# Performance work log

Measured on AMD Instinct MI355X. Metric: run time of the kernel, lower is better.

Reference implementation:

```python
import jax, jax.numpy as jnp
import numpy as np

N_NODES = 100000
N_EDGES = 1600000
D = 128          # in_channels // 4
IN_CH = 512
OUT_CH = 256
NUM_LABELS = 4


def setup_inputs() -> dict:
    key = jax.random.key(0)
    k1, k2, k3, k4, k5, k6 = jax.random.split(key, 6)
    x = jax.random.normal(k1, (N_NODES, D), dtype=jnp.float32)
    edge_index = jax.random.randint(k2, (2, N_EDGES), 0, N_NODES, dtype=jnp.int64)
    edge_label = jax.random.uniform(k3, (N_EDGES, NUM_LABELS), dtype=jnp.float32)
    # Parameters (uniform init per module's reset_parameters)
    stdv_w = 1.0 / np.sqrt(IN_CH)
    stdv_t = 1.0 / np.sqrt(NUM_LABELS)
    weight = jax.random.uniform(k4, (IN_CH, OUT_CH), minval=-stdv_w, maxval=stdv_w, dtype=jnp.float32)
    trans_weight = jax.random.uniform(k5, (NUM_LABELS, D), minval=-stdv_t, maxval=stdv_t, dtype=jnp.float32)
    bias = jax.random.uniform(k6, (OUT_CH,), minval=-stdv_w, maxval=stdv_w, dtype=jnp.float32)
    return {"x": x, "edge_index": edge_index, "edge_label": edge_label,
            "weight": weight, "trans_weight": trans_weight, "bias": bias}


def _scatter_mean(vals, idx, num_segments):
    # segment mean; empty segments -> 0 (matches torch_scatter.scatter_mean)
    s = jax.ops.segment_sum(vals, idx, num_segments=num_segments)
    cnt = jax.ops.segment_sum(jnp.ones((vals.shape[0],), dtype=vals.dtype), idx,
                              num_segments=num_segments)
    return s / jnp.maximum(cnt, 1.0)[:, None]


def reference(x, edge_index, edge_label, weight, trans_weight, bias):
    row, col = edge_index[0], edge_index[1]
    n = x.shape[0]
    # edge-label transform: [E, L] @ [L, D] -> [E, D]
    elt = jnp.matmul(edge_label, trans_weight)
    opinion = _scatter_mean(elt, row, n)        # outgoing opinion aggregation
    out = _scatter_mean(x[col], row, n)          # outgoing neighbor features
    inn_opinion = _scatter_mean(elt, col, n)     # incoming opinion aggregation
    inn = _scatter_mean(x[row], col, n)          # incoming neighbor features
    h = jnp.concatenate((out, opinion, inn, inn_opinion), axis=1)  # [N, 4D]
    return jnp.matmul(h, weight) + bias
```

## Files before the change

kernel.cpp:

```cpp
#include <hip/hip_runtime.h>
#include <hip/hip_bf16.h>


#define BK 64
#define BKSH 6
#define CHUNK 4096
#define CAPSEG 2048
#define CSSH 11
#define NB_CVT 256

typedef unsigned short u16;
typedef unsigned long long u64;
typedef __attribute__((ext_vector_type(4))) float f32x4;
typedef __attribute__((ext_vector_type(8))) short bf16x8;

__device__ inline unsigned pk_bf16(float a, float b) {
    __hip_bfloat162 h;
    h.x = __float2bfloat16(a);
    h.y = __float2bfloat16(b);
    return *reinterpret_cast<unsigned*>(&h);
}
__device__ inline float2 upk_bf16(unsigned u) {
    __hip_bfloat162 h = *reinterpret_cast<__hip_bfloat162*>(&u);
    return make_float2(__bfloat162float(h.x), __bfloat162float(h.y));
}
__device__ inline u16 f2bf(float f) {
    __hip_bfloat16 h = __float2bfloat16(f);
    return *reinterpret_cast<u16*>(&h);
}

__global__ __launch_bounds__(256) void cvt_bin(
    const float2* __restrict__ x2, unsigned* __restrict__ xh,
    const int* __restrict__ eidx, const float4* __restrict__ elab4,
    int* __restrict__ cnt_r, int* __restrict__ cnt_c,
    uint2* __restrict__ ent_r, uint2* __restrict__ ent_c,
    const float* __restrict__ w, const float* __restrict__ tw,
    u16* __restrict__ wb, int n2, int E, int nbk, int nchunk)
{
    __shared__ int smem[2048];
    const int t = threadIdx.x;
    const unsigned bid = blockIdx.x;

    if (bid < 2u * nchunk) {
        int* cB = smem;
        const int dir = (bid >= (unsigned)nchunk);
        const int base = (dir ? bid - nchunk : bid) * CHUNK;
        const int* __restrict__ osrc = eidx + (dir ? (size_t)E : 0);
        const int* __restrict__ psrc = eidx + (dir ? 0 : (size_t)E);
        int* __restrict__ cnt = dir ? cnt_c : cnt_r;
        uint2* __restrict__ ent = dir ? ent_c : ent_r;

        for (int i = t; i < nbk; i += 256) cB[i] = 0;
        __syncthreads();

        int4 own4[4], par4[4];
        unsigned lq[16];
        bool ok[4];
        #pragma unroll
        for (int jj = 0; jj < 4; ++jj) {
            const int e0 = base + (jj * 256 + t) * 4;
            ok[jj] = (e0 < E);
            if (ok[jj]) {
                own4[jj] = *(const int4*)(osrc + e0);
                par4[jj] = *(const int4*)(psrc + e0);
                #pragma unroll
                for (int k = 0; k < 4; ++k) {
                    const float4 lb = elab4[e0 + k];
                    const unsigned q0 = (unsigned)(lb.x * 255.f + 0.5f);
                    const unsigned q1 = (unsigned)(lb.y * 255.f + 0.5f);
                    const unsigned q2 = (unsigned)(lb.z * 255.f + 0.5f);
                    const unsigned q3 = (unsigned)(lb.w * 255.f + 0.5f);
                    lq[jj * 4 + k] = q0 | (q1 << 8) | (q2 << 16) | (q3 << 24);
                }
                atomicAdd(&cB[((unsigned)own4[jj].x) >> BKSH], 1);
                atomicAdd(&cB[((unsigned)own4[jj].y) >> BKSH], 1);
                atomicAdd(&cB[((unsigned)own4[jj].z) >> BKSH], 1);
                atomicAdd(&cB[((unsigned)own4[jj].w) >> BKSH], 1);
            }
        }
        __syncthreads();
        for (int b = t; b < nbk; b += 256) {
            const int c = cB[b];
            cB[b] = c ? ((b << CSSH) + atomicAdd(&cnt[b], c)) : 0;
        }
        __syncthreads();
        #pragma unroll
        for (int jj = 0; jj < 4; ++jj) {
            if (ok[jj]) {
                const int owns[4] = {own4[jj].x, own4[jj].y, own4[jj].z, own4[jj].w};
                const int pars[4] = {par4[jj].x, par4[jj].y, par4[jj].z, par4[jj].w};
                #pragma unroll
                for (int k = 0; k < 4; ++k) {
                    const unsigned own = (unsigned)owns[k];
                    const int p = atomicAdd(&cB[own >> BKSH], 1);
                    ent[p] = make_uint2((unsigned)pars[k] | ((own & (BK - 1u)) << 17),
                                        lq[jj * 4 + k]);
                }
            }
        }
        return;
    }

    if (bid < 2u * nchunk + NB_CVT) {
        const int cb = bid - 2 * nchunk;
        const int gsz = NB_CVT * 256;
        for (int i = cb * 256 + t; i < n2; i += gsz) {
            const float2 v = x2[i];
            xh[i] = pk_bf16(v.x, v.y);
        }
        return;
    }

    float (*P)[256] = (float(*)[256])smem;
    const int pid0 = (bid - 2 * nchunk - NB_CVT) * 256;
    if (pid0 + 255 >= 8192) {
        for (int q = t; q < 2048; q += 256) {
            const int l = q >> 8;
            const int cidx = q & 255;
            const int lr = l & 3;
            const int off = (l < 4) ? 128 : 384;
            float s = 0.f;
            for (int c = 0; c < 128; ++c)
                s = fmaf(tw[lr * 128 + c], w[(size_t)(off + c) * 256 + cidx], s);
            P[l][cidx] = s;
        }
        __syncthreads();
    }
    const int pid = pid0 + t;
    if (pid >= 9 * 16 * 64) return;
    const int ks = pid >> 10;
    const int ct = (pid >> 6) & 15;
    const int l  = pid & 63;
    const int col = ct * 16 + (l & 15);
    const int k0 = ks * 32 + ((l >> 4) << 3);
    u16 v[8];
    #pragma unroll
    for (int j = 0; j < 8; ++j) {
        const int k = k0 + j;
        float f = 0.f;
        if (k < 128)      f = w[(size_t)k * 256 + col];
        else if (k < 256) f = w[(size_t)(k + 128) * 256 + col];
        else if (k < 264) f = P[k - 256][col];
        v[j] = f2bf(f);
    }
    *(uint4*)(wb + (size_t)pid * 8) = *(uint4*)v;
}

__device__ inline void addrow(float* acc, const uint4 r) {
    const float2 a = upk_bf16(r.x), b = upk_bf16(r.y),
                 c = upk_bf16(r.z), d = upk_bf16(r.w);
    acc[0] += a.x; acc[1] += a.y; acc[2] += b.x; acc[3] += b.y;
    acc[4] += c.x; acc[5] += c.y; acc[6] += d.x; acc[7] += d.y;
}

__global__ __launch_bounds__(256) void sort_accum(
    const uint2* __restrict__ ent1_r, const uint2* __restrict__ ent1_c,
    const int* __restrict__ cnt_r, const int* __restrict__ cnt_c,
    const uint4* __restrict__ xh4,
    uint4* __restrict__ om4, uint4* __restrict__ im4,
    u16* __restrict__ lab_h, int nn, int nbk)
{
    __shared__ unsigned sorted[CAPSEG];
    __shared__ int hist[BK], sc[BK], curs[BK];
    __shared__ u64 labacc[BK];
    const int t = threadIdx.x;
    const int dir = (blockIdx.x >= (unsigned)nbk);
    const int b = blockIdx.x - (dir ? nbk : 0);
    const uint2* __restrict__ buf1 = (dir ? ent1_c : ent1_r) + ((size_t)b << CSSH);
    uint4* __restrict__ mean4 = dir ? im4 : om4;
    int cnt = (dir ? cnt_c : cnt_r)[b];
    if (cnt > CAPSEG) cnt = CAPSEG;

    if (t < BK) { hist[t] = 0; labacc[t] = 0ull; }
    __syncthreads();
    for (int i = t; i < cnt; i += 256) {
        const uint2 en = buf1[i];
        const unsigned local = en.x >> 17;
        atomicAdd(&hist[local], 1);
        const unsigned lv = en.y;
        const u64 spread = (u64)(lv & 255u) | ((u64)((lv >> 8) & 255u) << 16)
                         | ((u64)((lv >> 16) & 255u) << 32) | ((u64)(lv >> 24) << 48);
        atomicAdd(&labacc[local], spread);
    }
    __syncthreads();
    if (t < BK) sc[t] = hist[t];
    __syncthreads();
    for (int s = 1; s < BK; s <<= 1) {
        int v = 0;
        if (t < BK && t >= s) v = sc[t - s];
        __syncthreads();
        if (t < BK) sc[t] += v;
        __syncthreads();
    }
    if (t < BK) {
        curs[t] = sc[t] - hist[t];
        const int gn = b * BK + t;
        if (gn < nn) {
            const u64 sv = labacc[t];
            const float inv = (1.f / 255.f) / fmaxf((float)hist[t], 1.f);
            u16 lm[4];
            #pragma unroll
            for (int l = 0; l < 4; ++l)
                lm[l] = f2bf((float)((sv >> (16 * l)) & 0xFFFFu) * inv);
            *(uint2*)(lab_h + (size_t)gn * 8 + dir * 4) = *(uint2*)lm;
        }
    }
    __syncthreads();
    for (int i = t; i < cnt; i += 256) {
        const uint2 en = buf1[i];
        const int p = atomicAdd(&curs[en.x >> 17], 1);
        sorted[p] = en.x & 0x1FFFFu;
    }
    __syncthreads();

    const int wid = t >> 6;
    const int lane = t & 63;
    const int g = lane >> 4;
    const int sl = lane & 15;
    for (int local = wid; local < BK; local += 4) {
        const int gn = b * BK + local;
        if (gn >= nn) continue;
        const int segC = hist[local];
        const int segS = sc[local] - segC;
        float acc[8] = {0.f, 0.f, 0.f, 0.f, 0.f, 0.f, 0.f, 0.f};
        for (int i = 0; i < segC; i += 16) {
            const int rem = segC - i;
            const bool h0 = (g < rem);
            const bool h1 = (g + 4 < rem);
            const bool h2 = (g + 8 < rem);
            const bool h3 = (g + 12 < rem);
            const unsigned p0 = h0 ? sorted[segS + i + g] : 0u;
            const unsigned p1 = h1 ? sorted[segS + i + 4 + g] : 0u;
            const unsigned p2 = h2 ? sorted[segS + i + 8 + g] : 0u;
            const unsigned p3 = h3 ? sorted[segS + i + 12 + g] : 0u;
            uint4 r0, r1, r2, r3;
            if (h0) r0 = xh4[(size_t)p0 * 16 + sl];
            if (h1) r1 = xh4[(size_t)p1 * 16 + sl];
            if (h2) r2 = xh4[(size_t)p2 * 16 + sl];
            if (h3) r3 = xh4[(size_t)p3 * 16 + sl];
            if (h0) addrow(acc, r0);
            if (h1) addrow(acc, r1);
            if (h2) addrow(acc, r2);
            if (h3) addrow(acc, r3);
        }
        #pragma unroll
        for (int j = 0; j < 8; ++j) {
            acc[j] += __shfl_xor(acc[j], 16);
            acc[j] += __shfl_xor(acc[j], 32);
        }
        if (g == 0) {
            const float inv = 1.0f / fmaxf((float)segC, 1.0f);
            uint4 o;
            o.x = pk_bf16(acc[0] * inv, acc[1] * inv);
            o.y = pk_bf16(acc[2] * inv, acc[3] * inv);
            o.z = pk_bf16(acc[4] * inv, acc[5] * inv);
            o.w = pk_bf16(acc[6] * inv, acc[7] * inv);
            mean4[(size_t)gn * 16 + sl] = o;
        }
    }
}

__global__ __launch_bounds__(256) void gemm_mfma(
    const u16* __restrict__ om_h, const u16* __restrict__ im_h,
    const u16* __restrict__ lab_h, const u16* __restrict__ wb,
    const float* __restrict__ bias, float* __restrict__ out, int nn)
{
    const int t = threadIdx.x;
    const int w = t >> 6;
    const int lane = t & 63;
    const int m15 = lane & 15;
    const int kq  = lane >> 4;
    const int node0 = blockIdx.x * 64;

    f32x4 acc[4][4];
    #pragma unroll
    for (int i = 0; i < 4; ++i)
        #pragma unroll
        for (int j = 0; j < 4; ++j)
            acc[i][j] = (f32x4){0.f, 0.f, 0.f, 0.f};

    for (int ks = 0; ks < 9; ++ks) {
        const int k0 = ks * 32 + kq * 8;
        bf16x8 af[4], bfr[4];
        #pragma unroll
        for (int nt = 0; nt < 4; ++nt) {
            const int gn = node0 + nt * 16 + m15;
            bf16x8 a = (bf16x8){0, 0, 0, 0, 0, 0, 0, 0};
            if (gn < nn && k0 < 264) {
                const u16* p = (k0 < 128) ? om_h + (size_t)gn * 128 + k0
                             : (k0 < 256) ? im_h + (size_t)gn * 128 + (k0 - 128)
                                          : lab_h + (size_t)gn * 8;
                a = *(const bf16x8*)p;
            }
            af[nt] = a;
        }
        #pragma unroll
        for (int c2 = 0; c2 < 4; ++c2)
            bfr[c2] = *(const bf16x8*)(wb + ((size_t)((ks * 16 + w * 4 + c2) * 64 + lane)) * 8);
        #pragma unroll
        for (int nt = 0; nt < 4; ++nt)
            #pragma unroll
            for (int c2 = 0; c2 < 4; ++c2)
                acc[nt][c2] = __builtin_amdgcn_mfma_f32_16x16x32_bf16(
                    af[nt], bfr[c2], acc[nt][c2], 0, 0, 0);
    }

    #pragma unroll
    for (int nt = 0; nt < 4; ++nt) {
        const int gnb = node0 + nt * 16 + kq * 4;
        #pragma unroll
        for (int c2 = 0; c2 < 4; ++c2) {
            const int oc = w * 64 + c2 * 16 + m15;
            const float bv = bias[oc];
            #pragma unroll
            for (int r = 0; r < 4; ++r) {
                const int gn = gnb + r;
                if (gn < nn)
                    __builtin_nontemporal_store(acc[nt][c2][r] + bv,
                                                &out[(size_t)gn * 256 + oc]);
            }
        }
    }
}

extern "C" void kernel_launch(void* const* d_in, const int* in_sizes, int n_in,
                              void* d_out, int out_size, void* d_ws, size_t ws_size,
                              hipStream_t stream) {
    const float* x      = (const float*)d_in[0];
    const int*   eidx   = (const int*)d_in[1];
    const float* elabel = (const float*)d_in[2];
    const float* weight = (const float*)d_in[3];
    const float* tw     = (const float*)d_in[4];
    const float* bias   = (const float*)d_in[5];

    const int n = in_sizes[0] / 128;
    const int E = in_sizes[2] / 4;
    const int nbk = (n + BK - 1) / BK;
    const int nchunk = (E + CHUNK - 1) / CHUNK;

    char* wsb = (char*)d_ws;
    u16* om_h    = (u16*)wsb;   wsb += (size_t)n * 256;
    u16* im_h    = (u16*)wsb;   wsb += (size_t)n * 256;
    u16* lab_h   = (u16*)wsb;   wsb += (size_t)n * 16;
    u16* wb      = (u16*)wsb;   wsb += 9216 * 16;
    int* cnt_r   = (int*)wsb;   wsb += nbk * 4;
    int* cnt_c   = (int*)wsb;   wsb += nbk * 4;

    unsigned* xh = (unsigned*)d_out;
    uint2* ent1_r = (uint2*)(xh + (size_t)n * 64);
    uint2* ent1_c = ent1_r + ((size_t)nbk << CSSH);

    hipMemsetAsync(cnt_r, 0, (size_t)2 * nbk * sizeof(int), stream);

    hipLaunchKernelGGL(cvt_bin, dim3(2 * nchunk + NB_CVT + 36), dim3(256), 0, stream,
                       (const float2*)x, xh, eidx, (const float4*)elabel,
                       cnt_r, cnt_c, ent1_r, ent1_c,
                       weight, tw, wb, n * 64, E, nbk, nchunk);

    hipLaunchKernelGGL(sort_accum, dim3(2 * nbk), dim3(256), 0, stream,
                       ent1_r, ent1_c, cnt_r, cnt_c, (const uint4*)xh,
                       (uint4*)om_h, (uint4*)im_h, lab_h, n, nbk);

    hipLaunchKernelGGL(gemm_mfma, dim3((n + 63) / 64), dim3(256), 0, stream,
                       om_h, im_h, lab_h, wb, bias, (float*)d_out, n);
}
```

Before: 271.7 us.

## Fuse sort-accumulate and MFMA GEMM into one kernel via LDS staging

Merges the segment-mean aggregation kernel and the GEMM kernel into a single kernel. Each block now handles both edge directions for its 64 nodes, keeps the bf16 means and label means in shared memory, and then runs the MFMA GEMM straight from LDS. This removes the global write and re-read of the om/im/lab intermediates and one kernel launch. In exchange it halves the grid, serializes the two directions within a block, and raises LDS use, which can lower occupancy. Scratch buffers move from the output buffer to the workspace because the output is now written in the same kernel.

```diff
diff --git a/kernel.cpp b/kernel.cpp
--- a/kernel.cpp
+++ b/kernel.cpp
@@ -8,6 +8,7 @@
 #define CAPSEG 2048
 #define CSSH 11
 #define NB_CVT 256
+#define LDM 136
 
 typedef unsigned short u16;
 typedef unsigned long long u64;
@@ -153,125 +154,120 @@
     acc[4] += c.x; acc[5] += c.y; acc[6] += d.x; acc[7] += d.y;
 }
 
-__global__ __launch_bounds__(256) void sort_accum(
+__global__ __launch_bounds__(256) void sag(
     const uint2* __restrict__ ent1_r, const uint2* __restrict__ ent1_c,
     const int* __restrict__ cnt_r, const int* __restrict__ cnt_c,
-    const uint4* __restrict__ xh4,
-    uint4* __restrict__ om4, uint4* __restrict__ im4,
-    u16* __restrict__ lab_h, int nn, int nbk)
+    const uint4* __restrict__ xh4, const u16* __restrict__ wb,
+    const float* __restrict__ bias, float* __restrict__ out, int nn)
 {
     __shared__ unsigned sorted[CAPSEG];
     __shared__ int hist[BK], sc[BK], curs[BK];
     __shared__ u64 labacc[BK];
+    __shared__ u16 om_lds[BK * LDM];
+    __shared__ u16 im_lds[BK * LDM];
+    __shared__ u16 lab_lds[BK * 8];
     const int t = threadIdx.x;
-    const int dir = (blockIdx.x >= (unsigned)nbk);
-    const int b = blockIdx.x - (dir ? nbk : 0);
-    const uint2* __restrict__ buf1 = (dir ? ent1_c : ent1_r) + ((size_t)b << CSSH);
-    uint4* __restrict__ mean4 = dir ? im4 : om4;
-    int cnt = (dir ? cnt_c : cnt_r)[b];
-    if (cnt > CAPSEG) cnt = CAPSEG;
-
-    if (t < BK) { hist[t] = 0; labacc[t] = 0ull; }
-    __syncthreads();
-    for (int i = t; i < cnt; i += 256) {
-        const uint2 en = buf1[i];
-        const unsigned local = en.x >> 17;
-        atomicAdd(&hist[local], 1);
-        const unsigned lv = en.y;
-        const u64 spread = (u64)(lv & 255u) | ((u64)((lv >> 8) & 255u) << 16)
-                         | ((u64)((lv >> 16) & 255u) << 32) | ((u64)(lv >> 24) << 48);
-        atomicAdd(&labacc[local], spread);
-    }
-    __syncthreads();
-    if (t < BK) sc[t] = hist[t];
-    __syncthreads();
-    for (int s = 1; s < BK; s <<= 1) {
-        int v = 0;
-        if (t < BK && t >= s) v = sc[t - s];
-        __syncthreads();
-        if (t < BK) sc[t] += v;
-        __syncthreads();
-    }
-    if (t < BK) {
-        curs[t] = sc[t] - hist[t];
-        const int gn = b * BK + t;
-        if (gn < nn) {
-            const u64 sv = labacc[t];
-            const float inv = (1.f / 255.f) / fmaxf((float)hist[t], 1.f);
-            u16 lm[4];
-            #pragma unroll
-            for (int l = 0; l < 4; ++l)
-                lm[l] = f2bf((float)((sv >> (16 * l)) & 0xFFFFu) * inv);
-            *(uint2*)(lab_h + (size_t)gn * 8 + dir * 4) = *(uint2*)lm;
-        }
-    }
-    __syncthreads();
-    for (int i = t; i < cnt; i += 256) {
-        const uint2 en = buf1[i];
-        const int p = atomicAdd(&curs[en.x >> 17], 1);
-        sorted[p] = en.x & 0x1FFFFu;
-    }
-    __syncthreads();
-
+    const int b = blockIdx.x;
     const int wid = t >> 6;
     const int lane = t & 63;
     const int g = lane >> 4;
     const int sl = lane & 15;
-    for (int local = wid; local < BK; local += 4) {
-        const int gn = b * BK + local;
-        if (gn >= nn) continue;
-        const int segC = hist[local];
-        const int segS = sc[local] - segC;
-        float acc[8] = {0.f, 0.f, 0.f, 0.f, 0.f, 0.f, 0.f, 0.f};
-        for (int i = 0; i < segC; i += 16) {
-            const int rem = segC - i;
-            const bool h0 = (g < rem);
-            const bool h1 = (g + 4 < rem);
-            const bool h2 = (g + 8 < rem);
-            const bool h3 = (g + 12 < rem);
-            const unsigned p0 = h0 ? sorted[segS + i + g] : 0u;
-            const unsigned p1 = h1 ? sorted[segS + i + 4 + g] : 0u;
-            const unsigned p2 = h2 ? sorted[segS + i + 8 + g] : 0u;
-            const unsigned p3 = h3 ? sorted[segS + i + 12 + g] : 0u;
-            uint4 r0, r1, r2, r3;
-            if (h0) r0 = xh4[(size_t)p0 * 16 + sl];
-            if (h1) r1 = xh4[(size_t)p1 * 16 + sl];
-            if (h2) r2 = xh4[(size_t)p2 * 16 + sl];
-            if (h3) r3 = xh4[(size_t)p3 * 16 + sl];
-            if (h0) addrow(acc, r0);
-            if (h1) addrow(acc, r1);
-            if (h2) addrow(acc, r2);
-            if (h3) addrow(acc, r3);
-        }
-        #pragma unroll
-        for (int j = 0; j < 8; ++j) {
-            acc[j] += __shfl_xor(acc[j], 16);
-            acc[j] += __shfl_xor(acc[j], 32);
-        }
-        if (g == 0) {
-            const float inv = 1.0f / fmaxf((float)segC, 1.0f);
-            uint4 o;
-            o.x = pk_bf16(acc[0] * inv, acc[1] * inv);
-            o.y = pk_bf16(acc[2] * inv, acc[3] * inv);
-            o.z = pk_bf16(acc[4] * inv, acc[5] * inv);
-            o.w = pk_bf16(acc[6] * inv, acc[7] * inv);
-            mean4[(size_t)gn * 16 + sl] = o;
-        }
-    }
-}
-
-__global__ __launch_bounds__(256) void gemm_mfma(
-    const u16* __restrict__ om_h, const u16* __restrict__ im_h,
-    const u16* __restrict__ lab_h, const u16* __restrict__ wb,
-    const float* __restrict__ bias, float* __restrict__ out, int nn)
-{
-    const int t = threadIdx.x;
-    const int w = t >> 6;
-    const int lane = t & 63;
+    const int node0 = b * BK;
+
+    for (int dir = 0; dir < 2; ++dir) {
+        const uint2* __restrict__ buf1 = (dir ? ent1_c : ent1_r) + ((size_t)b << CSSH);
+        u16* __restrict__ mean_lds = dir ? im_lds : om_lds;
+        int cnt = (dir ? cnt_c : cnt_r)[b];
+        if (cnt > CAPSEG) cnt = CAPSEG;
+
+        if (t < BK) { hist[t] = 0; labacc[t] = 0ull; }
+        __syncthreads();
+        for (int i = t; i < cnt; i += 256) {
+            const uint2 en = buf1[i];
+            const unsigned local = en.x >> 17;
+            atomicAdd(&hist[local], 1);
+            const unsigned lv = en.y;
+            const u64 spread = (u64)(lv & 255u) | ((u64)((lv >> 8) & 255u) << 16)
+                             | ((u64)((lv >> 16) & 255u) << 32) | ((u64)(lv >> 24) << 48);
+            atomicAdd(&labacc[local], spread);
+        }
+        __syncthreads();
+        if (t < BK) sc[t] = hist[t];
+        __syncthreads();
+        for (int s = 1; s < BK; s <<= 1) {
+            int v = 0;
+            if (t < BK && t >= s) v = sc[t - s];
+            __syncthreads();
+            if (t < BK) sc[t] += v;
+            __syncthreads();
+        }
+        if (t < BK) {
+            curs[t] = sc[t] - hist[t];
+            const int gn = node0 + t;
+            if (gn < nn) {
+                const u64 sv = labacc[t];
+                const float inv = (1.f / 255.f) / fmaxf((float)hist[t], 1.f);
+                u16 lm[4];
+                #pragma unroll
+                for (int l = 0; l < 4; ++l)
+                    lm[l] = f2bf((float)((sv >> (16 * l)) & 0xFFFFu) * inv);
+                *(uint2*)(&lab_lds[t * 8 + dir * 4]) = *(uint2*)lm;
+            }
+        }
+        __syncthreads();
+        for (int i = t; i < cnt; i += 256) {
+            const uint2 en = buf1[i];
+            const int p = atomicAdd(&curs[en.x >> 17], 1);
+            sorted[p] = en.x & 0x1FFFFu;
+        }
+        __syncthreads();
+
+        for (int local = wid; local < BK; local += 4) {
+            const int gn = node0 + local;
+            if (gn >= nn) continue;
+            const int segC = hist[local];
+            const int segS = sc[local] - segC;
+            float acc[8] = {0.f, 0.f, 0.f, 0.f, 0.f, 0.f, 0.f, 0.f};
+            for (int i = 0; i < segC; i += 16) {
+                const int rem = segC - i;
+                const bool h0 = (g < rem);
+                const bool h1 = (g + 4 < rem);
+                const bool h2 = (g + 8 < rem);
+                const bool h3 = (g + 12 < rem);
+                const unsigned p0 = h0 ? sorted[segS + i + g] : 0u;
+                const unsigned p1 = h1 ? sorted[segS + i + 4 + g] : 0u;
+                const unsigned p2 = h2 ? sorted[segS + i + 8 + g] : 0u;
+                const unsigned p3 = h3 ? sorted[segS + i + 12 + g] : 0u;
+                uint4 r0, r1, r2, r3;
+                if (h0) r0 = xh4[(size_t)p0 * 16 + sl];
+                if (h1) r1 = xh4[(size_t)p1 * 16 + sl];
+                if (h2) r2 = xh4[(size_t)p2 * 16 + sl];
+                if (h3) r3 = xh4[(size_t)p3 * 16 + sl];
+                if (h0) addrow(acc, r0);
+                if (h1) addrow(acc, r1);
+                if (h2) addrow(acc, r2);
+                if (h3) addrow(acc, r3);
+            }
+            #pragma unroll
+            for (int j = 0; j < 8; ++j) {
+                acc[j] += __shfl_xor(acc[j], 16);
+                acc[j] += __shfl_xor(acc[j], 32);
+            }
+            if (g == 0) {
+                const float inv = 1.0f / fmaxf((float)segC, 1.0f);
+                uint4 o;
+                o.x = pk_bf16(acc[0] * inv, acc[1] * inv);
+                o.y = pk_bf16(acc[2] * inv, acc[3] * inv);
+                o.z = pk_bf16(acc[4] * inv, acc[5] * inv);
+                o.w = pk_bf16(acc[6] * inv, acc[7] * inv);
+                *(uint4*)(&mean_lds[local * LDM + sl * 8]) = o;
+            }
+        }
+        __syncthreads();
+    }
+
     const int m15 = lane & 15;
     const int kq  = lane >> 4;
-    const int node0 = blockIdx.x * 64;
-
     f32x4 acc[4][4];
     #pragma unroll
     for (int i = 0; i < 4; ++i)
@@ -284,19 +280,18 @@
         bf16x8 af[4], bfr[4];
         #pragma unroll
         for (int nt = 0; nt < 4; ++nt) {
-            const int gn = node0 + nt * 16 + m15;
+            const int row = nt * 16 + m15;
             bf16x8 a = (bf16x8){0, 0, 0, 0, 0, 0, 0, 0};
-            if (gn < nn && k0 < 264) {
-                const u16* p = (k0 < 128) ? om_h + (size_t)gn * 128 + k0
-                             : (k0 < 256) ? im_h + (size_t)gn * 128 + (k0 - 128)
-                                          : lab_h + (size_t)gn * 8;
-                a = *(const bf16x8*)p;
+            if (k0 < 264) {
+                if (k0 < 128)      a = *(const bf16x8*)(&om_lds[row * LDM + k0]);
+                else if (k0 < 256) a = *(const bf16x8*)(&im_lds[row * LDM + (k0 - 128)]);
+                else               a = *(const bf16x8*)(&lab_lds[row * 8]);
             }
             af[nt] = a;
         }
         #pragma unroll
         for (int c2 = 0; c2 < 4; ++c2)
-            bfr[c2] = *(const bf16x8*)(wb + ((size_t)((ks * 16 + w * 4 + c2) * 64 + lane)) * 8);
+            bfr[c2] = *(const bf16x8*)(wb + ((size_t)((ks * 16 + wid * 4 + c2) * 64 + lane)) * 8);
         #pragma unroll
         for (int nt = 0; nt < 4; ++nt)
             #pragma unroll
@@ -310,7 +305,7 @@
         const int gnb = node0 + nt * 16 + kq * 4;
         #pragma unroll
         for (int c2 = 0; c2 < 4; ++c2) {
-            const int oc = w * 64 + c2 * 16 + m15;
+            const int oc = wid * 64 + c2 * 16 + m15;
             const float bv = bias[oc];
             #pragma unroll
             for (int r = 0; r < 4; ++r) {
@@ -339,16 +334,12 @@
     const int nchunk = (E + CHUNK - 1) / CHUNK;
 
     char* wsb = (char*)d_ws;
-    u16* om_h    = (u16*)wsb;   wsb += (size_t)n * 256;
-    u16* im_h    = (u16*)wsb;   wsb += (size_t)n * 256;
-    u16* lab_h   = (u16*)wsb;   wsb += (size_t)n * 16;
-    u16* wb      = (u16*)wsb;   wsb += 9216 * 16;
-    int* cnt_r   = (int*)wsb;   wsb += nbk * 4;
-    int* cnt_c   = (int*)wsb;   wsb += nbk * 4;
-
-    unsigned* xh = (unsigned*)d_out;
-    uint2* ent1_r = (uint2*)(xh + (size_t)n * 64);
-    uint2* ent1_c = ent1_r + ((size_t)nbk << CSSH);
+    unsigned* xh  = (unsigned*)wsb;  wsb += (size_t)n * 256;
+    uint2* ent1_r = (uint2*)wsb;     wsb += ((size_t)nbk << CSSH) * 8;
+    uint2* ent1_c = (uint2*)wsb;     wsb += ((size_t)nbk << CSSH) * 8;
+    u16* wb       = (u16*)wsb;       wsb += 9216 * 16;
+    int* cnt_r    = (int*)wsb;       wsb += nbk * 4;
+    int* cnt_c    = (int*)wsb;       wsb += nbk * 4;
 
     hipMemsetAsync(cnt_r, 0, (size_t)2 * nbk * sizeof(int), stream);
 
@@ -357,10 +348,7 @@
                        cnt_r, cnt_c, ent1_r, ent1_c,
                        weight, tw, wb, n * 64, E, nbk, nchunk);
 
-    hipLaunchKernelGGL(sort_accum, dim3(2 * nbk), dim3(256), 0, stream,
+    hipLaunchKernelGGL(sag, dim3(nbk), dim3(256), 0, stream,
                        ent1_r, ent1_c, cnt_r, cnt_c, (const uint4*)xh,
-                       (uint4*)om_h, (uint4*)im_h, lab_h, n, nbk);
-
-    hipLaunchKernelGGL(gemm_mfma, dim3((n + 63) / 64), dim3(256), 0, stream,
-                       om_h, im_h, lab_h, wb, bias, (float*)d_out, n);
-}
+                       wb, bias, (float*)d_out, n);
+}
```

Result: slower. 350.0 us (+28.8%).

## Fuse GEMM into sort_accum via per-bucket completion flags, double bucket size

Applied to the files above, without the earlier changes.

Doubles the node bucket size (BK 64→128, segment capacity 2048→4096) and fuses the final MFMA GEMM into the sort/accumulate kernel. Each bucket's two direction blocks increment an atomic flag, and the second one to finish runs the GEMM for that bucket's 128 nodes. Staging buffers move from the output buffer into workspace when there is room, so output writes cannot clobber entries still being read. This removes a kernel launch and lets the GEMM overlap the scatter phase. The costs are fewer, larger sort blocks with more shared memory and a tail imbalance. It also relies on a fence and flag protocol, and `wid`/`lane` must be defined in the hidden part of sort_accum.

```diff
diff --git a/kernel.cpp b/kernel.cpp
--- a/kernel.cpp
+++ b/kernel.cpp
@@ -2,11 +2,11 @@
 #include <hip/hip_bf16.h>
 
 
-#define BK 64
-#define BKSH 6
+#define BK 128
+#define BKSH 7
 #define CHUNK 4096
-#define CAPSEG 2048
-#define CSSH 11
+#define CAPSEG 4096
+#define CSSH 12
 #define NB_CVT 256
 
 typedef unsigned short u16;
@@ -153,16 +153,78 @@
     acc[4] += c.x; acc[5] += c.y; acc[6] += d.x; acc[7] += d.y;
 }
 
+__device__ inline void gemm_tile(
+    int node0, const u16* __restrict__ om_h, const u16* __restrict__ im_h,
+    const u16* __restrict__ lab_h, const u16* __restrict__ wb,
+    const float* __restrict__ bias, float* __restrict__ out, int nn,
+    int wid, int lane)
+{
+    const int m15 = lane & 15;
+    const int kq  = lane >> 4;
+    f32x4 acc[4][4];
+    #pragma unroll
+    for (int i = 0; i < 4; ++i)
+        #pragma unroll
+        for (int j = 0; j < 4; ++j)
+            acc[i][j] = (f32x4){0.f, 0.f, 0.f, 0.f};
+
+    for (int ks = 0; ks < 9; ++ks) {
+        const int k0 = ks * 32 + kq * 8;
+        bf16x8 af[4], bfr[4];
+        #pragma unroll
+        for (int nt = 0; nt < 4; ++nt) {
+            const int gn = node0 + nt * 16 + m15;
+            bf16x8 a = (bf16x8){0, 0, 0, 0, 0, 0, 0, 0};
+            if (gn < nn && k0 < 264) {
+                const u16* p = (k0 < 128) ? om_h + (size_t)gn * 128 + k0
+                             : (k0 < 256) ? im_h + (size_t)gn * 128 + (k0 - 128)
+                                          : lab_h + (size_t)gn * 8;
+                a = *(const bf16x8*)p;
+            }
+            af[nt] = a;
+        }
+        #pragma unroll
+        for (int c2 = 0; c2 < 4; ++c2)
+            bfr[c2] = *(const bf16x8*)(wb + ((size_t)((ks * 16 + wid * 4 + c2) * 64 + lane)) * 8);
+        #pragma unroll
+        for (int nt = 0; nt < 4; ++nt)
+            #pragma unroll
+            for (int c2 = 0; c2 < 4; ++c2)
+                acc[nt][c2] = __builtin_amdgcn_mfma_f32_16x16x32_bf16(
+                    af[nt], bfr[c2], acc[nt][c2], 0, 0, 0);
+    }
+
+    #pragma unroll
+    for (int nt = 0; nt < 4; ++nt) {
+        const int gnb = node0 + nt * 16 + kq * 4;
+        #pragma unroll
+        for (int c2 = 0; c2 < 4; ++c2) {
+            const int oc = wid * 64 + c2 * 16 + m15;
+            const float bv = bias[oc];
+            #pragma unroll
+            for (int r = 0; r < 4; ++r) {
+                const int gn = gnb + r;
+                if (gn < nn)
+                    __builtin_nontemporal_store(acc[nt][c2][r] + bv,
+                                                &out[(size_t)gn * 256 + oc]);
+            }
+        }
+    }
+}
+
 __global__ __launch_bounds__(256) void sort_accum(
     const uint2* __restrict__ ent1_r, const uint2* __restrict__ ent1_c,
     const int* __restrict__ cnt_r, const int* __restrict__ cnt_c,
     const uint4* __restrict__ xh4,
     uint4* __restrict__ om4, uint4* __restrict__ im4,
-    u16* __restrict__ lab_h, int nn, int nbk)
+    u16* __restrict__ lab_h, int* __restrict__ flags,
+    const u16* __restrict__ wb, const float* __restrict__ bias,
+    float* __restrict__ out, int nn, int nbk, int fuse)
 {
     __shared__ unsigned sorted[CAPSEG];
     __shared__ int hist[BK], sc[BK], curs[BK];
     __shared__ u64 labacc[BK];
+    __shared__ int sflag;
     const int t = threadIdx.x;
     const int dir = (blockIdx.x >= (unsigned)nbk);
     const int b = blockIdx.x - (dir ? nbk : 0);
@@ -258,6 +320,22 @@
             mean4[(size_t)gn * 16 + sl] = o;
         }
     }
+
+    if (!fuse) return;
+
+    __syncthreads();
+    if (t == 0) {
+        __threadfence();
+        sflag = atomicAdd(&flags[b], 1);
+    }
+    __syncthreads();
+    if (sflag == 1) {
+        __threadfence();
+        gemm_tile(b * BK,      (const u16*)om4, (const u16*)im4, lab_h, wb,
+                  bias, out, nn, wid, lane);
+        gemm_tile(b * BK + 64, (const u16*)om4, (const u16*)im4, lab_h, wb,
+                  bias, out, nn, wid, lane);
+    }
 }
 
 __global__ __launch_bounds__(256) void gemm_mfma(
@@ -265,62 +343,8 @@
     const u16* __restrict__ lab_h, const u16* __restrict__ wb,
     const float* __restrict__ bias, float* __restrict__ out, int nn)
 {
-    const int t = threadIdx.x;
-    const int w = t >> 6;
-    const int lane = t & 63;
-    const int m15 = lane & 15;
-    const int kq  = lane >> 4;
-    const int node0 = blockIdx.x * 64;
-
-    f32x4 acc[4][4];
-    #pragma unroll
-    for (int i = 0; i < 4; ++i)
-        #pragma unroll
-        for (int j = 0; j < 4; ++j)
-            acc[i][j] = (f32x4){0.f, 0.f, 0.f, 0.f};
-
-    for (int ks = 0; ks < 9; ++ks) {
-        const int k0 = ks * 32 + kq * 8;
-        bf16x8 af[4], bfr[4];
-        #pragma unroll
-        for (int nt = 0; nt < 4; ++nt) {
-            const int gn = node0 + nt * 16 + m15;
-            bf16x8 a = (bf16x8){0, 0, 0, 0, 0, 0, 0, 0};
-            if (gn < nn && k0 < 264) {
-                const u16* p = (k0 < 128) ? om_h + (size_t)gn * 128 + k0
-                             : (k0 < 256) ? im_h + (size_t)gn * 128 + (k0 - 128)
-                                          : lab_h + (size_t)gn * 8;
-                a = *(const bf16x8*)p;
-            }
-            af[nt] = a;
-        }
-        #pragma unroll
-        for (int c2 = 0; c2 < 4; ++c2)
-            bfr[c2] = *(const bf16x8*)(wb + ((size_t)((ks * 16 + w * 4 + c2) * 64 + lane)) * 8);
-        #pragma unroll
-        for (int nt = 0; nt < 4; ++nt)
-            #pragma unroll
-            for (int c2 = 0; c2 < 4; ++c2)
-                acc[nt][c2] = __builtin_amdgcn_mfma_f32_16x16x32_bf16(
-                    af[nt], bfr[c2], acc[nt][c2], 0, 0, 0);
-    }
-
-    #pragma unroll
-    for (int nt = 0; nt < 4; ++nt) {
-        const int gnb = node0 + nt * 16 + kq * 4;
-        #pragma unroll
-        for (int c2 = 0; c2 < 4; ++c2) {
-            const int oc = w * 64 + c2 * 16 + m15;
-            const float bv = bias[oc];
-            #pragma unroll
-            for (int r = 0; r < 4; ++r) {
-                const int gn = gnb + r;
-                if (gn < nn)
-                    __builtin_nontemporal_store(acc[nt][c2][r] + bv,
-                                                &out[(size_t)gn * 256 + oc]);
-            }
-        }
-    }
+    gemm_tile(blockIdx.x * 64, om_h, im_h, lab_h, wb, bias, out, nn,
+              threadIdx.x >> 6, threadIdx.x & 63);
 }
 
 extern "C" void kernel_launch(void* const* d_in, const int* in_sizes, int n_in,
@@ -339,18 +363,23 @@
     const int nchunk = (E + CHUNK - 1) / CHUNK;
 
     char* wsb = (char*)d_ws;
-    u16* om_h    = (u16*)wsb;   wsb += (size_t)n * 256;
-    u16* im_h    = (u16*)wsb;   wsb += (size_t)n * 256;
-    u16* lab_h   = (u16*)wsb;   wsb += (size_t)n * 16;
-    u16* wb      = (u16*)wsb;   wsb += 9216 * 16;
-    int* cnt_r   = (int*)wsb;   wsb += nbk * 4;
-    int* cnt_c   = (int*)wsb;   wsb += nbk * 4;
-
-    unsigned* xh = (unsigned*)d_out;
-    uint2* ent1_r = (uint2*)(xh + (size_t)n * 64);
+    u16* om_h  = (u16*)wsb;  wsb += (size_t)n * 256;
+    u16* im_h  = (u16*)wsb;  wsb += (size_t)n * 256;
+    u16* lab_h = (u16*)wsb;  wsb += (size_t)n * 16;
+    u16* wb    = (u16*)wsb;  wsb += 9216 * 16;
+    int* cnt_r = (int*)wsb;  wsb += nbk * 4;
+    int* cnt_c = (int*)wsb;  wsb += nbk * 4;
+    int* flags = (int*)wsb;  wsb += nbk * 4;
+
+    const size_t staging_bytes = (size_t)n * 256 + 2 * (((size_t)nbk << CSSH) * 8);
+    const size_t used = (size_t)(wsb - (char*)d_ws);
+    const int fuse = (used + staging_bytes <= ws_size) ? 1 : 0;
+    char* stg = fuse ? wsb : (char*)d_out;
+    unsigned* xh  = (unsigned*)stg;
+    uint2* ent1_r = (uint2*)(stg + (size_t)n * 256);
     uint2* ent1_c = ent1_r + ((size_t)nbk << CSSH);
 
-    hipMemsetAsync(cnt_r, 0, (size_t)2 * nbk * sizeof(int), stream);
+    hipMemsetAsync(cnt_r, 0, (size_t)3 * nbk * sizeof(int), stream);
 
     hipLaunchKernelGGL(cvt_bin, dim3(2 * nchunk + NB_CVT + 36), dim3(256), 0, stream,
                        (const float2*)x, xh, eidx, (const float4*)elabel,
@@ -359,8 +388,10 @@
 
     hipLaunchKernelGGL(sort_accum, dim3(2 * nbk), dim3(256), 0, stream,
                        ent1_r, ent1_c, cnt_r, cnt_c, (const uint4*)xh,
-                       (uint4*)om_h, (uint4*)im_h, lab_h, n, nbk);
-
-    hipLaunchKernelGGL(gemm_mfma, dim3((n + 63) / 64), dim3(256), 0, stream,
-                       om_h, im_h, lab_h, wb, bias, (float*)d_out, n);
-}
+                       (uint4*)om_h, (uint4*)im_h, lab_h, flags,
+                       wb, bias, (float*)d_out, n, nbk, fuse);
+
+    if (!fuse)
+        hipLaunchKernelGGL(gemm_mfma, dim3((n + 63) / 64), dim3(256), 0, stream,
+                           om_h, im_h, lab_h, wb, bias, (float*)d_out, n);
+}
```

New measurement: 807.3 us. +197.1%, slower.
